# Performance work log

Measured on AMD Instinct MI355X. Metric: run time of the kernel, lower is better.

The kernel has to match this reference:

```python
import jax, jax.numpy as jnp
import numpy as np

N_NODES, N_EDGES, HIDDEN, N_GRAPHS = 100000, 500000, 128, 2048
ATOM_DIM, BOND_DIM, OUT_DIM = 4, 3, 1


def setup_inputs() -> dict:
    key = jax.random.key(0)
    ks = jax.random.split(key, 13)
    s = 0.05  # small init scale to keep relu+scatter depth iterations numerically tame
    return {
        "x": jax.random.normal(ks[0], (N_NODES, ATOM_DIM), jnp.float32),
        "edge_index": jax.random.randint(ks[1], (2, N_EDGES), 0, N_NODES, dtype=jnp.int32),
        "edge_attr": jax.random.normal(ks[2], (N_EDGES, BOND_DIM), jnp.float32),
        "batch": jnp.sort(jax.random.randint(ks[3], (N_NODES,), 0, N_GRAPHS, dtype=jnp.int32)),
        "depth": 3,
        # DMPNN weights (bias=False)
        "W_i": jax.random.normal(ks[4], (HIDDEN, ATOM_DIM + BOND_DIM), jnp.float32) * s,
        "W_m": jax.random.normal(ks[5], (HIDDEN, HIDDEN), jnp.float32) * s,
        "W_a": jax.random.normal(ks[6], (HIDDEN, ATOM_DIM + HIDDEN), jnp.float32) * s,
        # FFN: Linear(d,4d) -> relu -> dropout(eval=identity) -> Linear(4d,d)
        "W1": jax.random.normal(ks[7], (4 * HIDDEN, HIDDEN), jnp.float32) * s,
        "b1": jnp.zeros((4 * HIDDEN,), jnp.float32),
        "W2": jax.random.normal(ks[8], (HIDDEN, 4 * HIDDEN), jnp.float32) * s,
        "b2": jnp.zeros((HIDDEN,), jnp.float32),
        "W_last": jax.random.normal(ks[9], (OUT_DIM, HIDDEN), jnp.float32) * s,
        "b_last": jnp.zeros((OUT_DIM,), jnp.float32),
    }


def reference(x, edge_index, edge_attr, batch, depth, W_i, W_m, W_a, W1, b1, W2, b2, W_last, b_last):
    src, dst = edge_index[0], edge_index[1]
    E = edge_attr.shape[0]
    N = x.shape[0]
    # h: per-edge state [E, H]
    h = jax.nn.relu(jnp.concatenate([x[src], edge_attr], axis=1) @ W_i.T)
    for _ in range(depth):
        # message: relu(W_m h) gathered at src, scatter-add to dst; PyG infers
        # dim_size from h (edge-level here), so aggregation buffer has E rows.
        m = jax.nn.relu(h @ W_m.T)
        h = h + jax.ops.segment_sum(m[src], dst, num_segments=E)
    # index_add_ edge states to nodes
    node_emb = jax.ops.segment_sum(h, dst, num_segments=N)  # [N, H]
    node_emb = jax.nn.relu(jnp.concatenate([x, node_emb], axis=1) @ W_a.T)
    # global_add_pool over graphs
    g = jax.ops.segment_sum(node_emb, batch, num_segments=N_GRAPHS)  # [G, H]
    g = jax.nn.relu(g @ W1.T + b1) @ W2.T + b2  # FFN (dropout eval = identity)
    return g @ W_last.T + b_last  # [G, OUT_DIM]
```

## Files before the change

kernel.cpp:

```cpp
#include <hip/hip_runtime.h>


#define NN 100000
#define NE 500000
#define HID 128
#define NG 2048
#define NB_SCAN 391
#define NBLK256 391

typedef __attribute__((ext_vector_type(8))) short bf16x8;
typedef __attribute__((ext_vector_type(4))) float f32x4;

__device__ __forceinline__ float b2f(ushort u) {
  return __uint_as_float(((uint)u) << 16);
}
__device__ __forceinline__ ushort f2b(float f) {
  uint u = __float_as_uint(f);
  return (ushort)((u + 0x7FFF + ((u >> 16) & 1)) >> 16);
}
__device__ __forceinline__ void acc8(float* a, bf16x8 v) {
#pragma unroll
  for (int j = 0; j < 8; ++j) a[j] += b2f((ushort)v[j]);
}
__device__ __forceinline__ bf16x8 pack8(const float* a) {
  bf16x8 o;
#pragma unroll
  for (int j = 0; j < 8; ++j) o[j] = (short)f2b(a[j]);
  return o;
}
__device__ __forceinline__ size_t taddr(int n, int c8) {
  return ((size_t)(c8 >> 4) * NN + n) * 16 + (c8 & 8);
}

__global__ __launch_bounds__(256) void k_init_h8(const int* __restrict__ src,
    const float* __restrict__ x, const float* __restrict__ ea,
    const float* __restrict__ Wi, ushort* __restrict__ hT) {
  __shared__ float wis[HID * 7];
  for (int i = threadIdx.x; i < HID * 7; i += 256) wis[i] = Wi[i];
  __syncthreads();
  int idx = blockIdx.x * 256 + threadIdx.x;
  int e = idx >> 4, chunk = idx & 15;
  if (e >= NN) return;
  int s = src[e];
  float4 xv = *reinterpret_cast<const float4*>(&x[(size_t)s * 4]);
  float e0 = ea[(size_t)e*3+0], e1 = ea[(size_t)e*3+1], e2 = ea[(size_t)e*3+2];
  const float* w = &wis[chunk * 56];
  float a[8];
#pragma unroll
  for (int j = 0; j < 8; ++j) {
    const float* wj = &w[j * 7];
    float t = xv.x*wj[0] + xv.y*wj[1] + xv.z*wj[2] + xv.w*wj[3]
            + e0*wj[4] + e1*wj[5] + e2*wj[6];
    a[j] = fmaxf(t, 0.f);
  }
  *reinterpret_cast<bf16x8*>(&hT[((size_t)(chunk >> 1) * NN + e) * 16 + (chunk & 1) * 8]) = pack8(a);
}

__global__ __launch_bounds__(256) void k_hist2(const int* __restrict__ dst,
    int* __restrict__ cnt, int* __restrict__ cnt_lo) {
  int e = blockIdx.x * 256 + threadIdx.x;
  if (e >= NE) return;
  int d = dst[e];
  atomicAdd(&cnt[d], 1);
  if (e < NN) atomicAdd(&cnt_lo[d], 1);
}

__global__ __launch_bounds__(256) void k_scan1(const int* __restrict__ cnt,
    int* __restrict__ outp, int* __restrict__ bsums) {
  __shared__ int s[256];
  int t = threadIdx.x;
  int i = blockIdx.x * 256 + t;
  int v = (i < NN) ? cnt[i] : 0;
  s[t] = v;
  __syncthreads();
  for (int off = 1; off < 256; off <<= 1) {
    int u = (t >= off) ? s[t - off] : 0;
    __syncthreads();
    s[t] += u;
    __syncthreads();
  }
  if (i < NN) outp[i] = s[t] - v;
  if (t == 255) bsums[blockIdx.x] = s[255];
}

__global__ __launch_bounds__(512) void k_scan2(int* __restrict__ bsums) {
  __shared__ int s[512];
  int t = threadIdx.x;
  int v = (t < NB_SCAN) ? bsums[t] : 0;
  s[t] = v;
  __syncthreads();
  for (int off = 1; off < 512; off <<= 1) {
    int u = (t >= off) ? s[t - off] : 0;
    __syncthreads();
    s[t] += u;
    __syncthreads();
  }
  if (t < NB_SCAN) bsums[t] = s[t] - v;
}

__global__ __launch_bounds__(256) void k_scan3m(int* __restrict__ outp,
    const int* __restrict__ bsums, const int* __restrict__ cnt_lo,
    int* __restrict__ midp) {
  int i = blockIdx.x * 256 + threadIdx.x;
  if (i < NN) {
    int v = outp[i] + bsums[blockIdx.x];
    outp[i] = v;
    midp[i] = v + cnt_lo[i];
  }
  if (i == 0) outp[NN] = NE;
}

__global__ __launch_bounds__(256) void k_fill2z(const int* __restrict__ src,
    const int* __restrict__ dst, const int* __restrict__ rowptr,
    const int* __restrict__ midp, int* __restrict__ cur_lo,
    int* __restrict__ cur_hi, int* __restrict__ csr_src, int* __restrict__ csr_eid,
    const float* __restrict__ x, const float* __restrict__ ea,
    ushort* __restrict__ zpk) {
  int e = blockIdx.x * 256 + threadIdx.x;
  if (e >= NE) return;
  int d = dst[e];
  int s = src[e];
  int o;
  if (e < NN) {
    o = rowptr[d] + atomicAdd(&cur_lo[d], 1);
    csr_eid[o] = e;
  } else {
    o = midp[d] + atomicAdd(&cur_hi[d], 1);
    float4 xv = *reinterpret_cast<const float4*>(&x[(size_t)s * 4]);
    bf16x8 z;
    z[0] = (short)f2b(xv.x); z[1] = (short)f2b(xv.y);
    z[2] = (short)f2b(xv.z); z[3] = (short)f2b(xv.w);
    z[4] = (short)f2b(ea[(size_t)e*3+0]);
    z[5] = (short)f2b(ea[(size_t)e*3+1]);
    z[6] = (short)f2b(ea[(size_t)e*3+2]);
    z[7] = 0;
    *reinterpret_cast<bf16x8*>(&zpk[(size_t)o * 8]) = z;
  }
  csr_src[o] = s;
}

__global__ __launch_bounds__(256) void k_misc(const float* __restrict__ Wm,
    const float* __restrict__ Wa, ushort* __restrict__ wmb,
    ushort* __restrict__ wab, const int* __restrict__ batch,
    int* __restrict__ goff) {
  int gb = blockIdx.x;
  if (gb < 64) {
    int i = gb * 256 + threadIdx.x;
    wmb[i] = f2b(Wm[i]);
    int c = i >> 7, k = i & 127;
    wab[i] = f2b(Wa[c * 132 + 4 + k]);
  } else {
    int g = (gb - 64) * 256 + threadIdx.x;
    if (g > NG) return;
    int lo = 0, hi = NN;
    while (lo < hi) { int mid = (lo + hi) >> 1; if (batch[mid] < g) lo = mid + 1; else hi = mid; }
    goff[g] = lo;
  }
}

template <bool HASX>
__global__ __launch_bounds__(256) void k_mfma(const ushort* __restrict__ A,
    const ushort* __restrict__ Wb, const float* __restrict__ X,
    const float* __restrict__ WaF, ushort* __restrict__ O, int nrows) {
  int tid = threadIdx.x;
  int wave = tid >> 6;
  int lane = tid & 63;
  int wr = wave >> 1, wc = wave & 1;
  int row0 = blockIdx.x * 64 + wr * 32;
  int col0 = wc * 64;
  int l15 = lane & 15, l4 = lane >> 4;

  f32x4 acc[2][4];
#pragma unroll
  for (int mi = 0; mi < 2; ++mi)
#pragma unroll
    for (int ni = 0; ni < 4; ++ni) acc[mi][ni] = (f32x4){0.f, 0.f, 0.f, 0.f};

  if (HASX) {
    float4 wv[4];
#pragma unroll
    for (int ni = 0; ni < 4; ++ni)
      wv[ni] = *reinterpret_cast<const float4*>(&WaF[(size_t)(col0 + ni * 16 + l15) * 132]);
#pragma unroll
    for (int mi = 0; mi < 2; ++mi)
#pragma unroll
      for (int j = 0; j < 4; ++j) {
        int r = row0 + mi * 16 + l4 * 4 + j;
        if (r < nrows) {
          float4 xv = *reinterpret_cast<const float4*>(&X[(size_t)r * 4]);
#pragma unroll
          for (int ni = 0; ni < 4; ++ni)
            acc[mi][ni][j] = xv.x * wv[ni].x + xv.y * wv[ni].y
                           + xv.z * wv[ni].z + xv.w * wv[ni].w;
        }
      }
  }

  const bf16x8 zero8 = {0, 0, 0, 0, 0, 0, 0, 0};
#pragma unroll
  for (int k0 = 0; k0 < HID; k0 += 32) {
    bf16x8 a[2], b[4];
    int c8 = k0 + l4 * 8;
#pragma unroll
    for (int mi = 0; mi < 2; ++mi) {
      int r = row0 + mi * 16 + l15;
      a[mi] = (r < nrows)
            ? *reinterpret_cast<const bf16x8*>(&A[taddr(r, c8)])
            : zero8;
    }
#pragma unroll
    for (int ni = 0; ni < 4; ++ni) {
      int c = col0 + ni * 16 + l15;
      b[ni] = *reinterpret_cast<const bf16x8*>(&Wb[(size_t)c * HID + k0 + l4 * 8]);
    }
#pragma unroll
    for (int mi = 0; mi < 2; ++mi)
#pragma unroll
      for (int ni = 0; ni < 4; ++ni)
        acc[mi][ni] = __builtin_amdgcn_mfma_f32_16x16x32_bf16(a[mi], b[ni], acc[mi][ni], 0, 0, 0);
  }

#pragma unroll
  for (int mi = 0; mi < 2; ++mi)
#pragma unroll
    for (int j = 0; j < 4; ++j) {
      int r = row0 + mi * 16 + l4 * 4 + j;
      if (r >= nrows) continue;
#pragma unroll
      for (int ni = 0; ni < 4; ++ni) {
        int plane = wc * 4 + ni;
        O[((size_t)plane * NN + r) * 16 + l15] = f2b(fmaxf(acc[mi][ni][j], 0.f));
      }
    }
}

__global__ __launch_bounds__(256) void k_gather_x(const ushort* __restrict__ mT,
    const int* __restrict__ rowptr, const int* __restrict__ csr_src,
    ushort* __restrict__ hT) {
  int plane = blockIdx.x & 7;
  int nb = blockIdx.x >> 3;
  int n = nb * 256 + threadIdx.x;
  if (n >= NN) return;
  size_t pb = (size_t)plane * NN;
  size_t base = (pb + n) * 16;
  const bf16x8 zero8 = {0, 0, 0, 0, 0, 0, 0, 0};
  float a[16];
  bf16x8 h0 = *reinterpret_cast<const bf16x8*>(&hT[base]);
  bf16x8 h1 = *reinterpret_cast<const bf16x8*>(&hT[base + 8]);
#pragma unroll
  for (int j = 0; j < 8; ++j) { a[j] = b2f((ushort)h0[j]); a[8+j] = b2f((ushort)h1[j]); }
  int beg = rowptr[n], end = rowptr[n + 1];
  for (int i = beg; i < end; i += 4) {
    bf16x8 v0[4], v1[4];
#pragma unroll
    for (int k = 0; k < 4; ++k) {
      v0[k] = zero8; v1[k] = zero8;
      if (i + k < end) {
        size_t sb = (pb + csr_src[i + k]) * 16;
        v0[k] = *reinterpret_cast<const bf16x8*>(&mT[sb]);
        v1[k] = *reinterpret_cast<const bf16x8*>(&mT[sb + 8]);
      }
    }
#pragma unroll
    for (int k = 0; k < 4; ++k) { acc8(a, v0[k]); acc8(a + 8, v1[k]); }
  }
  *reinterpret_cast<bf16x8*>(&hT[base]) = pack8(a);
  *reinterpret_cast<bf16x8*>(&hT[base + 8]) = pack8(a + 8);
}

__global__ __launch_bounds__(256) void k_node_agg3(const ushort* __restrict__ hT,
    const int* __restrict__ rowptr, const int* __restrict__ midp,
    const int* __restrict__ csr_eid, const ushort* __restrict__ zpk,
    const float* __restrict__ Wi, ushort* __restrict__ neT) {
  int idx = blockIdx.x * 256 + threadIdx.x;
  int n = idx >> 4;
  int t = idx & 15;
  int plane = t >> 1;
  int half8 = (t & 1) * 8;
  int c8 = t * 8;
  float w[8][7];
#pragma unroll
  for (int j = 0; j < 8; ++j)
#pragma unroll
    for (int k = 0; k < 7; ++k) w[j][k] = Wi[(c8 + j) * 7 + k];
  if (n >= NN) return;
  size_t pb = (size_t)plane * NN;
  int beg = rowptr[n], mid = midp[n], end = rowptr[n + 1];
  const bf16x8 zero8 = {0, 0, 0, 0, 0, 0, 0, 0};
  float a[8];
#pragma unroll
  for (int j = 0; j < 8; ++j) a[j] = 0.f;

  for (int i = beg; i < mid; i += 4) {
    bf16x8 v[4];
#pragma unroll
    for (int k = 0; k < 4; ++k) {
      v[k] = zero8;
      if (i + k < mid) {
        int e = csr_eid[i + k];
        v[k] = *reinterpret_cast<const bf16x8*>(&hT[(pb + e) * 16 + half8]);
      }
    }
#pragma unroll
    for (int k = 0; k < 4; ++k) acc8(a, v[k]);
  }

  for (int i = mid; i < end; i += 4) {
    bf16x8 zv[4];
#pragma unroll
    for (int k = 0; k < 4; ++k) {
      zv[k] = zero8;
      if (i + k < end)
        zv[k] = *reinterpret_cast<const bf16x8*>(&zpk[(size_t)(i + k) * 8]);
    }
#pragma unroll
    for (int k = 0; k < 4; ++k) {
      if (i + k < end) {
        float z0 = b2f((ushort)zv[k][0]), z1 = b2f((ushort)zv[k][1]);
        float z2 = b2f((ushort)zv[k][2]), z3 = b2f((ushort)zv[k][3]);
        float z4 = b2f((ushort)zv[k][4]), z5 = b2f((ushort)zv[k][5]);
        float z6 = b2f((ushort)zv[k][6]);
#pragma unroll
        for (int j = 0; j < 8; ++j) {
          float tt = z0*w[j][0] + z1*w[j][1] + z2*w[j][2] + z3*w[j][3]
                   + z4*w[j][4] + z5*w[j][5] + z6*w[j][6];
          a[j] += fmaxf(tt, 0.f);
        }
      }
    }
  }
  *reinterpret_cast<bf16x8*>(&neT[(pb + n) * 16 + half8]) = pack8(a);
}

__global__ __launch_bounds__(256) void k_pool(const ushort* __restrict__ na,
    const int* __restrict__ goff, float* __restrict__ g) {
  int idx = blockIdx.x * 256 + threadIdx.x;
  int gid = idx >> 4;
  if (gid >= NG) return;
  int c8 = (idx & 15) * 8;
  size_t pbase = (size_t)(c8 >> 4) * NN;
  int off = c8 & 8;
  int beg = goff[gid], end = goff[gid + 1];
  float a[8];
#pragma unroll
  for (int j = 0; j < 8; ++j) a[j] = 0.f;
  for (int n = beg; n < end; ++n)
    acc8(a, *reinterpret_cast<const bf16x8*>(&na[(pbase + n) * 16 + off]));
  *reinterpret_cast<float4*>(&g[(size_t)gid * HID + c8]) = make_float4(a[0], a[1], a[2], a[3]);
  *reinterpret_cast<float4*>(&g[(size_t)gid * HID + c8 + 4]) = make_float4(a[4], a[5], a[6], a[7]);
}

template <bool RELU>
__global__ __launch_bounds__(256) void k_gemm64(const float* __restrict__ A,
    const float* __restrict__ W, const float* __restrict__ bias,
    float* __restrict__ O, int nrows, int K, int N) {
  __shared__ float As[64][33];
  __shared__ float Bs[32][68];
  int tid = threadIdx.x;
  int row0 = blockIdx.x * 64;
  int col0 = blockIdx.y * 64;
  int tn = tid & 15;
  int tm = tid >> 4;
  float acc[4][4];
#pragma unroll
  for (int i = 0; i < 4; ++i)
#pragma unroll
    for (int j = 0; j < 4; ++j) acc[i][j] = 0.f;

  for (int k0 = 0; k0 < K; k0 += 32) {
    int ar = tid >> 3;
    int ak = (tid & 7) << 2;
#pragma unroll
    for (int rr = 0; rr < 2; ++rr) {
      int r = row0 + ar + rr * 32;
      float4 v = make_float4(0.f, 0.f, 0.f, 0.f);
      if (r < nrows) v = *reinterpret_cast<const float4*>(&A[(size_t)r * K + k0 + ak]);
      As[ar + rr*32][ak+0] = v.x; As[ar + rr*32][ak+1] = v.y;
      As[ar + rr*32][ak+2] = v.z; As[ar + rr*32][ak+3] = v.w;
    }
    int c = tid & 63;
    int kq = tid >> 6;
#pragma unroll
    for (int it = 0; it < 2; ++it) {
      int kk = kq * 4 + it * 16;
      float4 v = *reinterpret_cast<const float4*>(&W[(size_t)(col0 + c) * K + k0 + kk]);
      Bs[kk+0][c] = v.x; Bs[kk+1][c] = v.y; Bs[kk+2][c] = v.z; Bs[kk+3][c] = v.w;
    }
    __syncthreads();
#pragma unroll 8
    for (int k = 0; k < 32; ++k) {
      float av[4];
#pragma unroll
      for (int i = 0; i < 4; ++i) av[i] = As[tm*4 + i][k];
      float4 bv = *reinterpret_cast<const float4*>(&Bs[k][tn*4]);
#pragma unroll
      for (int i = 0; i < 4; ++i) {
        acc[i][0] = fmaf(av[i], bv.x, acc[i][0]);
        acc[i][1] = fmaf(av[i], bv.y, acc[i][1]);
        acc[i][2] = fmaf(av[i], bv.z, acc[i][2]);
        acc[i][3] = fmaf(av[i], bv.w, acc[i][3]);
      }
    }
    __syncthreads();
  }
#pragma unroll
  for (int i = 0; i < 4; ++i) {
    int r = row0 + tm * 4 + i;
    if (r >= nrows) continue;
    float4 o;
    int c = col0 + tn * 4;
    o.x = acc[i][0] + bias[c+0];
    o.y = acc[i][1] + bias[c+1];
    o.z = acc[i][2] + bias[c+2];
    o.w = acc[i][3] + bias[c+3];
    if (RELU) {
      o.x = fmaxf(o.x, 0.f); o.y = fmaxf(o.y, 0.f);
      o.z = fmaxf(o.z, 0.f); o.w = fmaxf(o.w, 0.f);
    }
    *reinterpret_cast<float4*>(&O[(size_t)r * N + c]) = o;
  }
}

__global__ __launch_bounds__(256) void k_last(const float* __restrict__ g3,
    const float* __restrict__ Wl, const float* __restrict__ bl,
    float* __restrict__ out) {
  int wid = (blockIdx.x * 256 + threadIdx.x) >> 6;
  int lane = threadIdx.x & 63;
  if (wid >= NG) return;
  float a = g3[(size_t)wid*128 + lane] * Wl[lane]
          + g3[(size_t)wid*128 + 64 + lane] * Wl[64 + lane];
  for (int off = 32; off; off >>= 1) a += __shfl_down(a, off);
  if (lane == 0) out[wid] = a + bl[0];
}

extern "C" void kernel_launch(void* const* d_in, const int* in_sizes, int n_in,
                              void* d_out, int out_size, void* d_ws, size_t ws_size,
                              hipStream_t stream) {
  const float* x    = (const float*)d_in[0];
  const int*   eidx = (const int*)d_in[1];
  const float* ea   = (const float*)d_in[2];
  const int*   batch= (const int*)d_in[3];
  const float* Wi   = (const float*)d_in[5];
  const float* Wm   = (const float*)d_in[6];
  const float* Wa   = (const float*)d_in[7];
  const float* W1   = (const float*)d_in[8];
  const float* b1   = (const float*)d_in[9];
  const float* W2   = (const float*)d_in[10];
  const float* b2   = (const float*)d_in[11];
  const float* Wl   = (const float*)d_in[12];
  const float* bl   = (const float*)d_in[13];
  float* out = (float*)d_out;

  const int* src = eidx;
  const int* dst = eidx + NE;

  char* p = (char*)d_ws;
  ushort* hb  = (ushort*)p; p += (size_t)NN * HID * 2;
  ushort* mb  = (ushort*)p; p += (size_t)NN * HID * 2;
  ushort* wmb = (ushort*)p; p += (size_t)HID * HID * 2;
  ushort* wab = (ushort*)p; p += (size_t)HID * HID * 2;
  ushort* zpk = (ushort*)p; p += (size_t)NE * 8 * 2;
  float* g  = (float*)p; p += (size_t)NG * 128 * 4;
  float* g2 = (float*)p; p += (size_t)NG * 512 * 4;
  float* g3 = (float*)p; p += (size_t)NG * 128 * 4;
  int* csr_src = (int*)p; p += (size_t)NE * 4;
  int* csr_eid = (int*)p; p += (size_t)NE * 4;
  int* cnt    = (int*)p; p += (size_t)NN * 4;
  int* cnt_lo = (int*)p; p += (size_t)NN * 4;
  int* cur_lo = (int*)p; p += (size_t)NN * 4;
  int* cur_hi = (int*)p; p += (size_t)NN * 4;
  int* rowptr = (int*)p; p += (size_t)(NN + 4) * 4;
  int* midp   = (int*)p; p += (size_t)NN * 4;
  int* bsums  = (int*)p; p += 512 * 4;
  int* goff   = (int*)p; p += (size_t)(NG + 4) * 4;

  hipMemsetAsync(cnt, 0, (size_t)4 * NN * sizeof(int), stream);
  k_hist2<<<(NE + 255) / 256, 256, 0, stream>>>(dst, cnt, cnt_lo);
  k_scan1<<<NB_SCAN, 256, 0, stream>>>(cnt, rowptr, bsums);
  k_scan2<<<1, 512, 0, stream>>>(bsums);
  k_scan3m<<<NB_SCAN, 256, 0, stream>>>(rowptr, bsums, cnt_lo, midp);
  k_fill2z<<<(NE + 255) / 256, 256, 0, stream>>>(src, dst, rowptr, midp,
                                                 cur_lo, cur_hi, csr_src, csr_eid,
                                                 x, ea, zpk);
  k_misc<<<64 + 9, 256, 0, stream>>>(Wm, Wa, wmb, wab, batch, goff);

  k_init_h8<<<(NN * 16 + 255) / 256, 256, 0, stream>>>(src, x, ea, Wi, hb);

  int ggrid = (NN + 63) / 64;
  for (int it = 0; it < 3; ++it) {
    k_mfma<false><<<ggrid, 256, 0, stream>>>(hb, wmb, nullptr, nullptr, mb, NN);
    k_gather_x<<<8 * NBLK256, 256, 0, stream>>>(mb, rowptr, csr_src, hb);
  }

  k_node_agg3<<<(NN * 16 + 255) / 256, 256, 0, stream>>>(hb, rowptr, midp,
                                                         csr_eid, zpk, Wi, mb);
  k_mfma<true><<<ggrid, 256, 0, stream>>>(mb, wab, x, Wa, hb, NN);

  k_pool<<<(NG * 16 + 255) / 256, 256, 0, stream>>>(hb, goff, g);

  dim3 grid1((NG + 63) / 64, 512 / 64);
  k_gemm64<true><<<grid1, 256, 0, stream>>>(g, W1, b1, g2, NG, 128, 512);
  dim3 grid2((NG + 63) / 64, 128 / 64);
  k_gemm64<false><<<grid2, 256, 0, stream>>>(g2, W2, b2, g3, NG, 512, 128);
  k_last<<<(NG * 64) / 256, 256, 0, stream>>>(g3, Wl, bl, out);
}
```

Before: 439.2 us.

## Sort nodes by in-degree to balance warps in gather kernel

Adds a degree histogram, a descending scan and a placement kernel that build a permutation of nodes ordered by in-degree, which the per-node gather kernel then follows. Threads in a wavefront get similar loop trip counts, reducing divergence from variable-length neighbor lists. In exchange it adds three small kernels and an extra indirection, and the rows each wavefront reads and writes become scattered instead of contiguous, which hurts coalescing of the hT reads and writes.

```diff
diff --git a/kernel.cpp b/kernel.cpp
--- a/kernel.cpp
+++ b/kernel.cpp
@@ -108,6 +108,39 @@
     midp[i] = v + cnt_lo[i];
   }
   if (i == 0) outp[NN] = NE;
+}
+
+__global__ __launch_bounds__(256) void k_deghist(const int* __restrict__ rowptr,
+    int* __restrict__ bins) {
+  int n = blockIdx.x * 256 + threadIdx.x;
+  if (n >= NN) return;
+  int d = min(rowptr[n + 1] - rowptr[n], 255);
+  atomicAdd(&bins[d], 1);
+}
+
+__global__ __launch_bounds__(256) void k_degscan(int* __restrict__ bins) {
+  __shared__ int s[256];
+  int t = threadIdx.x;
+  int v = bins[255 - t];
+  s[t] = v;
+  __syncthreads();
+  for (int off = 1; off < 256; off <<= 1) {
+    int u = (t >= off) ? s[t - off] : 0;
+    __syncthreads();
+    s[t] += u;
+    __syncthreads();
+  }
+  bins[255 - t] = s[t] - v;
+}
+
+__global__ __launch_bounds__(256) void k_place(const int* __restrict__ rowptr,
+    const int* __restrict__ binoff, int* __restrict__ cursor,
+    int* __restrict__ perm) {
+  int n = blockIdx.x * 256 + threadIdx.x;
+  if (n >= NN) return;
+  int d = min(rowptr[n + 1] - rowptr[n], 255);
+  int pos = binoff[d] + atomicAdd(&cursor[d], 1);
+  perm[pos] = n;
 }
 
 __global__ __launch_bounds__(256) void k_fill2z(const int* __restrict__ src,
@@ -236,11 +269,12 @@
 
 __global__ __launch_bounds__(256) void k_gather_x(const ushort* __restrict__ mT,
     const int* __restrict__ rowptr, const int* __restrict__ csr_src,
-    ushort* __restrict__ hT) {
+    const int* __restrict__ perm, ushort* __restrict__ hT) {
   int plane = blockIdx.x & 7;
   int nb = blockIdx.x >> 3;
-  int n = nb * 256 + threadIdx.x;
-  if (n >= NN) return;
+  int idx = nb * 256 + threadIdx.x;
+  if (idx >= NN) return;
+  int n = perm[idx];
   size_t pb = (size_t)plane * NN;
   size_t base = (pb + n) * 16;
   const bf16x8 zero8 = {0, 0, 0, 0, 0, 0, 0, 0};
@@ -469,16 +503,22 @@
   int* cnt_lo = (int*)p; p += (size_t)NN * 4;
   int* cur_lo = (int*)p; p += (size_t)NN * 4;
   int* cur_hi = (int*)p; p += (size_t)NN * 4;
+  int* dbins  = (int*)p; p += 256 * 4;
+  int* dcur   = (int*)p; p += 256 * 4;
   int* rowptr = (int*)p; p += (size_t)(NN + 4) * 4;
   int* midp   = (int*)p; p += (size_t)NN * 4;
   int* bsums  = (int*)p; p += 512 * 4;
   int* goff   = (int*)p; p += (size_t)(NG + 4) * 4;
-
-  hipMemsetAsync(cnt, 0, (size_t)4 * NN * sizeof(int), stream);
+  int* perm   = (int*)p; p += (size_t)NN * 4;
+
+  hipMemsetAsync(cnt, 0, ((size_t)4 * NN + 512) * sizeof(int), stream);
   k_hist2<<<(NE + 255) / 256, 256, 0, stream>>>(dst, cnt, cnt_lo);
   k_scan1<<<NB_SCAN, 256, 0, stream>>>(cnt, rowptr, bsums);
   k_scan2<<<1, 512, 0, stream>>>(bsums);
   k_scan3m<<<NB_SCAN, 256, 0, stream>>>(rowptr, bsums, cnt_lo, midp);
+  k_deghist<<<NB_SCAN, 256, 0, stream>>>(rowptr, dbins);
+  k_degscan<<<1, 256, 0, stream>>>(dbins);
+  k_place<<<NB_SCAN, 256, 0, stream>>>(rowptr, dbins, dcur, perm);
   k_fill2z<<<(NE + 255) / 256, 256, 0, stream>>>(src, dst, rowptr, midp,
                                                  cur_lo, cur_hi, csr_src, csr_eid,
                                                  x, ea, zpk);
@@ -489,7 +529,7 @@
   int ggrid = (NN + 63) / 64;
   for (int it = 0; it < 3; ++it) {
     k_mfma<false><<<ggrid, 256, 0, stream>>>(hb, wmb, nullptr, nullptr, mb, NN);
-    k_gather_x<<<8 * NBLK256, 256, 0, stream>>>(mb, rowptr, csr_src, hb);
+    k_gather_x<<<8 * NBLK256, 256, 0, stream>>>(mb, rowptr, csr_src, perm, hb);
   }
 
   k_node_agg3<<<(NN * 16 + 255) / 256, 256, 0, stream>>>(hb, rowptr, midp,
```

After: 1.307 ms. 2.98x slower.
